# Optimization experiments

Measured on AMD Instinct MI355X. Metric: run time of the kernel, lower is better.

The kernel has to match this reference:

```python
import jax, jax.numpy as jnp
import numpy as np

VIS_DIM, TXT_DIM, HID = 2048, 1024, 1024


def setup_inputs() -> dict:
    key = jax.random.key(0)
    ks = jax.random.split(key, 8)
    def lin(kw, kb, fan_in, fan_out):
        bound = 1.0 / np.sqrt(fan_in)
        W = jax.random.uniform(kw, (fan_out, fan_in), jnp.float32, -bound, bound)
        b = jax.random.uniform(kb, (fan_out,), jnp.float32, -bound, bound)
        return W, b
    Wv, bv = lin(ks[0], ks[1], VIS_DIM, HID)
    Wt, bt = lin(ks[2], ks[3], TXT_DIM, HID)
    Wa, ba = lin(ks[4], ks[5], HID, 1)
    return {
        "visual_features": jax.random.normal(ks[6], (128, 256, VIS_DIM), jnp.float32),
        "text_features": jax.random.normal(ks[7], (128, TXT_DIM), jnp.float32),
        "Wv": Wv, "bv": bv, "Wt": Wt, "bt": bt, "Wa": Wa, "ba": ba,
    }


def reference(visual_features, text_features, Wv, bv, Wt, bt, Wa, ba):
    # v: (B, R, H); t: (B, 1, H) broadcast over regions
    v = jnp.einsum("brd,hd->brh", visual_features, Wv) + bv
    t = (text_features @ Wt.T + bt)[:, None, :]
    combined = jnp.tanh(v + t)                       # (B, R, H)
    scores = jnp.einsum("brh,h->br", combined, Wa[0]) + ba[0]  # (B, R)
    attention_weights = jax.nn.softmax(scores, axis=1)
    attended = jnp.einsum("br,brd->bd", attention_weights, visual_features)
    return attended, attention_weights
```

## Files before the change

kernel.cpp:

```cpp
#include <hip/hip_runtime.h>
#include <hip/hip_bf16.h>

#define VIS_DIM 2048
#define TXT_DIM 1024
#define HID     1024
#define NB      128
#define NR      256
#define M_TOT   (NB*NR)

#define N_ATILES 8192
#define N_TILES  8448
#define TILE_B   16384
#define TSTRIDE  (32 * TILE_B)
#define WS_SCORES_OFF ((size_t)N_TILES * TILE_B)
#define WS_NEED (WS_SCORES_OFF + 131072 + 524288)

typedef __attribute__((ext_vector_type(4))) float  f32x4;
typedef __attribute__((ext_vector_type(8))) short  short8;
typedef __attribute__((ext_vector_type(4))) unsigned short u16x4;

static __device__ __forceinline__ unsigned short f2bf(float f) {
    union { __hip_bfloat16 h; unsigned short u; } c;
    c.h = __float2bfloat16(f);
    return c.u;
}

static __device__ __forceinline__ float bf2f(unsigned short u) {
    union { float f; unsigned u; } c; c.u = ((unsigned)u) << 16; return c.f;
}

static __device__ __forceinline__ float tanh_fast(float x) {
    float xc = fminf(fmaxf(x, -15.f), 15.f);
    float e  = __expf(2.f * xc);
    return (e - 1.f) / (e + 1.f);
}

__global__ void init_ws(float* __restrict__ scores, float* __restrict__ tbuf,
                        const float* __restrict__ bt) {
    int i = blockIdx.x * 256 + threadIdx.x;
    if (i < M_TOT) scores[i] = 0.f;
    tbuf[i] = bt[i & (HID - 1)];
}

__global__ __launch_bounds__(256) void prepass(const float* __restrict__ A,
                                               const float* __restrict__ Bv,
                                               unsigned short* __restrict__ w16) {
    const int t   = blockIdx.x;
    const int tid = threadIdx.x;
    const int mb  = (t < N_ATILES ? t : t - N_ATILES) >> 5;
    const int kt  = t & 31;
    const float* src = (t < N_ATILES ? A : Bv) + (size_t)mb * 128 * VIS_DIM + kt * 64;
    unsigned short* dst = w16 + (size_t)t * (TILE_B / 2);
    #pragma unroll
    for (int i = 0; i < 4; ++i) {
        int si = i * 256 + tid;
        int row = si >> 3, slot = si & 7;
        const float* p = src + (size_t)row * VIS_DIM + slot * 8;
        f32x4 lo = *(const f32x4*)p;
        f32x4 hi = *(const f32x4*)(p + 4);
        short8 v;
        v[0] = (short)f2bf(lo.x); v[1] = (short)f2bf(lo.y);
        v[2] = (short)f2bf(lo.z); v[3] = (short)f2bf(lo.w);
        v[4] = (short)f2bf(hi.x); v[5] = (short)f2bf(hi.y);
        v[6] = (short)f2bf(hi.z); v[7] = (short)f2bf(hi.w);
        *(short8*)(dst + row * 64 + ((slot ^ (row & 7)) << 3)) = v;
    }
}

__global__ __launch_bounds__(256) void gemm_text(const float* __restrict__ text,
                                                 const float* __restrict__ Wt,
                                                 float* __restrict__ tbuf) {
    __shared__ float As[128][33];
    __shared__ float Bs[32][33];
    const int n0  = blockIdx.x * 32;
    const int k0  = blockIdx.y * 256;
    const int tid = threadIdx.x;
    const int tm  = tid >> 3;
    const int tn  = tid & 7;
    float acc[4][4] = {};
    for (int kt = 0; kt < 8; ++kt) {
        const int k = k0 + kt * 32;
        {
            int row = tid >> 1, off = (tid & 1) * 16;
            const float* src = text + row * TXT_DIM + k + off;
            #pragma unroll
            for (int j = 0; j < 4; ++j) {
                f32x4 v = *(const f32x4*)(src + j * 4);
                As[row][off + j*4 + 0] = v.x; As[row][off + j*4 + 1] = v.y;
                As[row][off + j*4 + 2] = v.z; As[row][off + j*4 + 3] = v.w;
            }
        }
        {
            int row = tid >> 3, off = (tid & 7) * 4;
            f32x4 v = *(const f32x4*)(Wt + (size_t)(n0 + row) * TXT_DIM + k + off);
            Bs[row][off + 0] = v.x; Bs[row][off + 1] = v.y;
            Bs[row][off + 2] = v.z; Bs[row][off + 3] = v.w;
        }
        __syncthreads();
        #pragma unroll
        for (int kk = 0; kk < 32; ++kk) {
            float a[4], b[4];
            #pragma unroll
            for (int i = 0; i < 4; ++i) a[i] = As[tm*4 + i][kk];
            #pragma unroll
            for (int j = 0; j < 4; ++j) b[j] = Bs[tn*4 + j][kk];
            #pragma unroll
            for (int i = 0; i < 4; ++i)
                #pragma unroll
                for (int j = 0; j < 4; ++j) acc[i][j] += a[i] * b[j];
        }
        __syncthreads();
    }
    #pragma unroll
    for (int i = 0; i < 4; ++i)
        #pragma unroll
        for (int j = 0; j < 4; ++j)
            atomicAdd(&tbuf[(tm*4 + i) * HID + n0 + tn*4 + j], acc[i][j]);
}

static __device__ __forceinline__ int toff(int row, int kElem) {
    return row * 128 + ((((kElem >> 3) & 7) ^ (row & 7)) << 4);
}

__global__ __launch_bounds__(512, 2) void gemm_256(
        const unsigned short* __restrict__ w16,
        const float* __restrict__ bv,
        const float* __restrict__ wa,
        const float* __restrict__ tbuf,
        float* __restrict__ scores) {
    __shared__ __align__(16) char lds[131072];

    const int wg   = blockIdx.x;
    const int xcd  = wg & 7;
    const int loc  = wg >> 3;
    const int mb   = xcd * 16 + (loc >> 2);
    const int nb   = loc & 3;
    const int brow = mb * 256;
    const int bcol = nb * 256;

    const int tid  = threadIdx.x;
    const int lane = tid & 63;
    const int wid  = tid >> 6;
    const int wr   = wid >> 2;
    const int wc   = wid & 3;
    const int l    = lane & 15, g = lane >> 4;

    const char* wb = (const char*)w16;
    const char* pA = wb + (size_t)(2 * mb) * TSTRIDE + wid * 1024 + lane * 16;
    const char* pB = wb + (size_t)N_ATILES * TILE_B
                        + (size_t)(2 * nb) * TSTRIDE + wid * 1024 + lane * 16;

    f32x4 acc[8][4] = {};

#define GLOADS(koff, bufbase)                                                  \
    do {                                                                       \
        _Pragma("unroll")                                                      \
        for (int j = 0; j < 8; ++j) {                                          \
            const char* s_ = (j < 4                                            \
                ? pA + (j >> 1) * (size_t)TSTRIDE + (j & 1) * 8192             \
                : pB + ((j - 4) >> 1) * (size_t)TSTRIDE + ((j - 4) & 1) * 8192)\
                + (koff);                                                      \
            __builtin_amdgcn_global_load_lds(                                  \
                (const __attribute__((address_space(1))) float*)s_,            \
                (__attribute__((address_space(3))) float*)                     \
                    (lds + (bufbase) + j * 8192 + wid * 1024),                 \
                16, 0, 0);                                                     \
        }                                                                      \
    } while (0)

#define VWAIT0()                                                               \
    do {                                                                       \
        __builtin_amdgcn_sched_barrier(0);                                     \
        asm volatile("s_waitcnt vmcnt(0)" ::: "memory");                       \
        __builtin_amdgcn_sched_barrier(0);                                     \
    } while (0)

#define BARRIER()                                                              \
    do {                                                                       \
        __builtin_amdgcn_sched_barrier(0);                                     \
        asm volatile("s_waitcnt lgkmcnt(0)" ::: "memory");                     \
        __builtin_amdgcn_s_barrier();                                          \
        __builtin_amdgcn_sched_barrier(0);                                     \
    } while (0)

#define PHASE(bufbase, s)                                                      \
    do {                                                                       \
        const int kE = (s) * 32 + g * 8;                                       \
        const char* pa_ = lds + (bufbase) + wr * 16384;                        \
        const char* pb_ = lds + (bufbase) + 32768 + (wc >> 1) * 16384;         \
        short8 bfr[4], afr[8];                                                 \
        _Pragma("unroll")                                                      \
        for (int n = 0; n < 4; ++n)                                            \
            bfr[n] = *(const short8*)(pb_ + toff((wc & 1) * 64 + n * 16 + l, kE)); \
        _Pragma("unroll")                                                      \
        for (int m = 0; m < 8; ++m)                                            \
            afr[m] = *(const short8*)(pa_ + toff(m * 16 + l, kE));             \
        __builtin_amdgcn_s_setprio(1);                                         \
        _Pragma("unroll")                                                      \
        for (int m = 0; m < 8; ++m) {                                          \
            acc[m][0] = __builtin_amdgcn_mfma_f32_16x16x32_bf16(afr[m], bfr[0], acc[m][0], 0, 0, 0); \
            acc[m][1] = __builtin_amdgcn_mfma_f32_16x16x32_bf16(afr[m], bfr[1], acc[m][1], 0, 0, 0); \
            acc[m][2] = __builtin_amdgcn_mfma_f32_16x16x32_bf16(afr[m], bfr[2], acc[m][2], 0, 0, 0); \
            acc[m][3] = __builtin_amdgcn_mfma_f32_16x16x32_bf16(afr[m], bfr[3], acc[m][3], 0, 0, 0); \
        }                                                                      \
        __builtin_amdgcn_s_setprio(0);                                         \
    } while (0)

    GLOADS((size_t)0, 0);
    VWAIT0();
    GLOADS((size_t)TILE_B, 65536);
    BARRIER();

    #pragma unroll 1
    for (int i = 0; i < 16; ++i) {
        const size_t k2 = (size_t)(2 * i + 2) * TILE_B;
        PHASE(0, 0);
        PHASE(0, 1);
        VWAIT0();
        BARRIER();
        if (i < 15) GLOADS(k2, 0);
        PHASE(65536, 0);
        PHASE(65536, 1);
        if (i < 15) {
            VWAIT0();
            BARRIER();
            GLOADS(k2 + TILE_B, 65536);
        }
    }
#undef GLOADS
#undef VWAIT0
#undef BARRIER
#undef PHASE

    const int b = mb;
    float wa_c[4], bvt_c[4];
    #pragma unroll
    for (int n = 0; n < 4; ++n) {
        int col = bcol + wc * 64 + n * 16 + l;
        wa_c[n]  = wa[col];
        bvt_c[n] = bv[col] + tbuf[b * HID + col];
    }
    #pragma unroll
    for (int m = 0; m < 8; ++m) {
        float p0 = 0.f, p1 = 0.f, p2 = 0.f, p3 = 0.f;
        #pragma unroll
        for (int n = 0; n < 4; ++n) {
            f32x4 v = acc[m][n];
            p0 += wa_c[n] * tanh_fast(v.x + bvt_c[n]);
            p1 += wa_c[n] * tanh_fast(v.y + bvt_c[n]);
            p2 += wa_c[n] * tanh_fast(v.z + bvt_c[n]);
            p3 += wa_c[n] * tanh_fast(v.w + bvt_c[n]);
        }
        #pragma unroll
        for (int d = 1; d < 16; d <<= 1) {
            p0 += __shfl_xor(p0, d); p1 += __shfl_xor(p1, d);
            p2 += __shfl_xor(p2, d); p3 += __shfl_xor(p3, d);
        }
        if ((lane & 15) == 0) {
            int rowg = brow + wr * 128 + m * 16 + g * 4;
            atomicAdd(&scores[rowg + 0], p0);
            atomicAdd(&scores[rowg + 1], p1);
            atomicAdd(&scores[rowg + 2], p2);
            atomicAdd(&scores[rowg + 3], p3);
        }
    }
}

__global__ __launch_bounds__(256) void attend_bf16(
        const unsigned short* __restrict__ w16,
        const float* __restrict__ scores,
        float* __restrict__ out) {
    const int chunk = blockIdx.x;
    const int b     = blockIdx.y;
    const int tid   = threadIdx.x;
    const int lane  = tid & 63;
    const int wv    = tid >> 6;

    __shared__ float wsm[NR];
    __shared__ float red[4];
    __shared__ float part2[4][32][8];

    float s = scores[b * NR + tid];
    float mx = s;
    #pragma unroll
    for (int d = 1; d < 64; d <<= 1) mx = fmaxf(mx, __shfl_xor(mx, d));
    if (lane == 0) red[wv] = mx;
    __syncthreads();
    mx = fmaxf(fmaxf(red[0], red[1]), fmaxf(red[2], red[3]));
    float e = __expf(s - mx);
    float sum = e;
    #pragma unroll
    for (int d = 1; d < 64; d <<= 1) sum += __shfl_xor(sum, d);
    __syncthreads();
    if (lane == 0) red[wv] = sum;
    __syncthreads();
    sum = red[0] + red[1] + red[2] + red[3];
    float w = e * (1.f / sum);
    wsm[tid] = w;
    if (chunk == 0) out[(size_t)NB * VIS_DIM + b * NR + tid] = w;
    __syncthreads();

    const int half  = lane >> 5;
    const int dslot = lane & 31;
    const int d0    = chunk * 256 + dslot * 8;
    const int kt    = d0 >> 6;
    const int ksl   = (d0 >> 3) & 7;
    const int rbase = b * 256 + wv * 64 + half;

    float acc[8] = {};
    #pragma unroll 4
    for (int step = 0; step < 32; ++step) {
        int rowg = rbase + step * 2;
        const char* p = (const char*)w16
            + ((size_t)(rowg >> 7) * 32 + kt) * TILE_B
            + (rowg & 127) * 128 + ((ksl ^ (rowg & 7)) << 4);
        short8 v = *(const short8*)p;
        float w_ = wsm[wv * 64 + step * 2 + half];
        #pragma unroll
        for (int j = 0; j < 8; ++j)
            acc[j] += w_ * bf2f((unsigned short)v[j]);
    }
    #pragma unroll
    for (int j = 0; j < 8; ++j) acc[j] += __shfl_xor(acc[j], 32);

    if (half == 0) {
        #pragma unroll
        for (int j = 0; j < 8; ++j) part2[wv][dslot][j] = acc[j];
    }
    __syncthreads();
    if (wv == 0 && half == 0) {
        float o[8];
        #pragma unroll
        for (int j = 0; j < 8; ++j)
            o[j] = part2[0][dslot][j] + part2[1][dslot][j]
                 + part2[2][dslot][j] + part2[3][dslot][j];
        float* dst = out + (size_t)b * VIS_DIM + chunk * 256 + dslot * 8;
        f32x4 lo = {o[0], o[1], o[2], o[3]};
        f32x4 hi = {o[4], o[5], o[6], o[7]};
        *(f32x4*)dst = lo;
        *(f32x4*)(dst + 4) = hi;
    }
}

#define BK 32
#define NT (VIS_DIM / BK)

static __device__ __forceinline__ int tile_off(int row, int kElem) {
    return row * 64 + (((kElem >> 3) ^ ((row >> 1) & 3)) << 4);
}

__global__ __launch_bounds__(256, 2) void gemm_vis(
        const float* __restrict__ A,
        const float* __restrict__ Bv,
        const float* __restrict__ bv,
        const float* __restrict__ wa,
        const float* __restrict__ tbuf,
        float* __restrict__ scores) {
    __shared__ __align__(16) char lds[32768];

    const int wg   = blockIdx.x;
    const int xcd  = wg & 7;
    const int loc  = wg >> 3;
    const int mb   = xcd * 32 + (loc >> 3);
    const int nb   = loc & 7;
    const int brow = mb * 128;
    const int bcol = nb * 128;

    const int tid  = threadIdx.x;
    const int lane = tid & 63;
    const int wid  = tid >> 6;
    const int wr   = wid >> 1, wc = wid & 1;

    const int srow = tid >> 3;
    const int sfs  = tid & 7;
    unsigned va0 = ((unsigned)(brow + srow      ) * VIS_DIM + sfs * 4) * 4u;
    unsigned va1 = va0 + 32u * VIS_DIM * 4u;
    unsigned va2 = va0 + 64u * VIS_DIM * 4u;
    unsigned va3 = va0 + 96u * VIS_DIM * 4u;
    unsigned vb0 = ((unsigned)(bcol + srow      ) * VIS_DIM + sfs * 4) * 4u;
    unsigned vb1 = vb0 + 32u * VIS_DIM * 4u;
    unsigned vb2 = vb0 + 64u * VIS_DIM * 4u;
    unsigned vb3 = vb0 + 96u * VIS_DIM * 4u;

    int wbyte[4];
    #pragma unroll
    for (int r = 0; r < 4; ++r) {
        int row = srow + 32 * r;
        wbyte[r] = row * 64 + (((sfs >> 1) ^ ((row >> 1) & 3)) << 4) + (sfs & 1) * 8;
    }

    f32x4 sA0, sA1, sA2, sA3, sB0, sB1, sB2, sB3;
    f32x4 tA0, tA1, tA2, tA3, tB0, tB1, tB2, tB3;
    f32x4 acc[4][4] = {};

#define GLOAD_SET(dA0,dA1,dA2,dA3,dB0,dB1,dB2,dB3)                             \
    do {                                                                       \
        asm volatile("global_load_dwordx4 %0, %1, %2"                          \
                     : "=&v"(dA0) : "v"(va0), "s"(A) : "memory");              \
        asm volatile("global_load_dwordx4 %0, %1, %2"                          \
                     : "=&v"(dA1) : "v"(va1), "s"(A) : "memory");              \
        asm volatile("global_load_dwordx4 %0, %1, %2"                          \
                     : "=&v"(dA2) : "v"(va2), "s"(A) : "memory");              \
        asm volatile("global_load_dwordx4 %0, %1, %2"                          \
                     : "=&v"(dA3) : "v"(va3), "s"(A) : "memory");              \
        asm volatile("global_load_dwordx4 %0, %1, %2"                          \
                     : "=&v"(dB0) : "v"(vb0), "s"(Bv) : "memory");             \
        asm volatile("global_load_dwordx4 %0, %1, %2"                          \
                     : "=&v"(dB1) : "v"(vb1), "s"(Bv) : "memory");             \
        asm volatile("global_load_dwordx4 %0, %1, %2"                          \
                     : "=&v"(dB2) : "v"(vb2), "s"(Bv) : "memory");             \
        asm volatile("global_load_dwordx4 %0, %1, %2"                          \
                     : "=&v"(dB3) : "v"(vb3), "s"(Bv) : "memory");             \
        va0 += BK * 4; va1 += BK * 4; va2 += BK * 4; va3 += BK * 4;            \
        vb0 += BK * 4; vb1 += BK * 4; vb2 += BK * 4; vb3 += BK * 4;            \
    } while (0)

#define GLOAD_S() GLOAD_SET(sA0,sA1,sA2,sA3,sB0,sB1,sB2,sB3)
#define GLOAD_T() GLOAD_SET(tA0,tA1,tA2,tA3,tB0,tB1,tB2,tB3)

#define VWAIT(N)                                                               \
    do {                                                                       \
        __builtin_amdgcn_sched_barrier(0);                                     \
        asm volatile("s_waitcnt vmcnt(" #N ")" ::: "memory");                  \
        __builtin_amdgcn_sched_barrier(0);                                     \
    } while (0)

#define BARRIER()                                                              \
    do {                                                                       \
        __builtin_amdgcn_sched_barrier(0);                                     \
        asm volatile("s_waitcnt lgkmcnt(0)" ::: "memory");                     \
        __builtin_amdgcn_s_barrier();                                          \
        __builtin_amdgcn_sched_barrier(0);                                     \
    } while (0)

#define CVT8(dst, v0)                                                          \
    do {                                                                       \
        u16x4 t_;                                                              \
        t_.x = f2bf((v0).x); t_.y = f2bf((v0).y);                              \
        t_.z = f2bf((v0).z); t_.w = f2bf((v0).w);                              \
        dst = t_;                                                              \
    } while (0)

#define LWRITE_SET(bufbase, dA0,dA1,dA2,dA3,dB0,dB1,dB2,dB3)                   \
    do {                                                                       \
        u16x4 w_;                                                              \
        char* la = lds + (bufbase);                                            \
        char* lb = lds + (bufbase) + 8192;                                     \
        CVT8(w_, dA0); *(u16x4*)(la + wbyte[0]) = w_;                          \
        CVT8(w_, dA1); *(u16x4*)(la + wbyte[1]) = w_;                          \
        CVT8(w_, dA2); *(u16x4*)(la + wbyte[2]) = w_;                          \
        CVT8(w_, dA3); *(u16x4*)(la + wbyte[3]) = w_;                          \
        CVT8(w_, dB0); *(u16x4*)(lb + wbyte[0]) = w_;                          \
        CVT8(w_, dB1); *(u16x4*)(lb + wbyte[1]) = w_;                          \
        CVT8(w_, dB2); *(u16x4*)(lb + wbyte[2]) = w_;                          \
        CVT8(w_, dB3); *(u16x4*)(lb + wbyte[3]) = w_;                          \
    } while (0)

#define LWRITE_S(bufbase) LWRITE_SET(bufbase, sA0,sA1,sA2,sA3,sB0,sB1,sB2,sB3)
#define LWRITE_T(bufbase) LWRITE_SET(bufbase, tA0,tA1,tA2,tA3,tB0,tB1,tB2,tB3)

#define COMPUTE(bufbase)                                                       \
    do {                                                                       \
        short8 af[4], bf[4];                                                   \
        const int kk = (lane >> 4) * 8;                                        \
        const char* la = lds + (bufbase);                                      \
        const char* lb = lds + (bufbase) + 8192;                               \
        _Pragma("unroll")                                                      \
        for (int m = 0; m < 4; ++m)                                            \
            af[m] = *(const short8*)(la + tile_off(wr*64 + m*16 + (lane&15), kk)); \
        _Pragma("unroll")                                                      \
        for (int n = 0; n < 4; ++n)                                            \
            bf[n] = *(const short8*)(lb + tile_off(wc*64 + n*16 + (lane&15), kk)); \
        _Pragma("unroll")                                                      \
        for (int m = 0; m < 4; ++m)                                            \
            _Pragma("unroll")                                                  \
            for (int n = 0; n < 4; ++n)                                        \
                acc[m][n] = __builtin_amdgcn_mfma_f32_16x16x32_bf16(           \
                    af[m], bf[n], acc[m][n], 0, 0, 0);                         \
    } while (0)

    GLOAD_S();
    GLOAD_T();
    VWAIT(8);
    LWRITE_S(0);
    BARRIER();

    #pragma unroll 1
    for (int kt = 0; kt < NT - 2; kt += 2) {
        GLOAD_S();
        COMPUTE(0);
        VWAIT(8);
        LWRITE_T(16384);
        BARRIER();
        GLOAD_T();
        COMPUTE(16384);
        VWAIT(8);
        LWRITE_S(0);
        BARRIER();
    }
    COMPUTE(0);
    VWAIT(0);
    LWRITE_T(16384);
    BARRIER();
    COMPUTE(16384);
#undef GLOAD_SET
#undef GLOAD_S
#undef GLOAD_T
#undef VWAIT
#undef BARRIER
#undef CVT8
#undef LWRITE_SET
#undef LWRITE_S
#undef LWRITE_T
#undef COMPUTE

    const int b = brow >> 8;
    float wa_c[4], bvt_c[4];
    #pragma unroll
    for (int n = 0; n < 4; ++n) {
        int col = bcol + wc * 64 + n * 16 + (lane & 15);
        wa_c[n]  = wa[col];
        bvt_c[n] = bv[col] + tbuf[b * HID + col];
    }
    #pragma unroll
    for (int m = 0; m < 4; ++m) {
        float p0 = 0.f, p1 = 0.f, p2 = 0.f, p3 = 0.f;
        #pragma unroll
        for (int n = 0; n < 4; ++n) {
            f32x4 v = acc[m][n];
            p0 += wa_c[n] * tanh_fast(v.x + bvt_c[n]);
            p1 += wa_c[n] * tanh_fast(v.y + bvt_c[n]);
            p2 += wa_c[n] * tanh_fast(v.z + bvt_c[n]);
            p3 += wa_c[n] * tanh_fast(v.w + bvt_c[n]);
        }
        #pragma unroll
        for (int d = 1; d < 16; d <<= 1) {
            p0 += __shfl_xor(p0, d); p1 += __shfl_xor(p1, d);
            p2 += __shfl_xor(p2, d); p3 += __shfl_xor(p3, d);
        }
        if ((lane & 15) == 0) {
            int rowg = brow + wr * 64 + m * 16 + (lane >> 4) * 4;
            atomicAdd(&scores[rowg + 0], p0);
            atomicAdd(&scores[rowg + 1], p1);
            atomicAdd(&scores[rowg + 2], p2);
            atomicAdd(&scores[rowg + 3], p3);
        }
    }
}

__global__ __launch_bounds__(256) void attend(const float* __restrict__ visual,
                                              const float* __restrict__ scores,
                                              float* __restrict__ out) {
    const int chunk = blockIdx.x;
    const int b     = blockIdx.y;
    const int tid   = threadIdx.x;
    const int lane  = tid & 63;
    const int wv    = tid >> 6;

    __shared__ float wsm[NR];
    __shared__ float red[4];
    __shared__ f32x4 part[4][64];

    float s = scores[b * NR + tid];
    float mx = s;
    #pragma unroll
    for (int d = 1; d < 64; d <<= 1) mx = fmaxf(mx, __shfl_xor(mx, d));
    if (lane == 0) red[wv] = mx;
    __syncthreads();
    mx = fmaxf(fmaxf(red[0], red[1]), fmaxf(red[2], red[3]));
    float e = __expf(s - mx);
    float sum = e;
    #pragma unroll
    for (int d = 1; d < 64; d <<= 1) sum += __shfl_xor(sum, d);
    __syncthreads();
    if (lane == 0) red[wv] = sum;
    __syncthreads();
    sum = red[0] + red[1] + red[2] + red[3];
    float w = e * (1.f / sum);
    wsm[tid] = w;
    if (chunk == 0) out[(size_t)NB * VIS_DIM + b * NR + tid] = w;
    __syncthreads();

    const float* vb = visual + ((size_t)b * NR + wv * 64) * VIS_DIM + chunk * 256 + lane * 4;
    f32x4 acc = {0.f, 0.f, 0.f, 0.f};
    #pragma unroll
    for (int r = 0; r < 64; r += 4) {
        f32x4 v0 = *(const f32x4*)(vb + (size_t)(r + 0) * VIS_DIM);
        f32x4 v1 = *(const f32x4*)(vb + (size_t)(r + 1) * VIS_DIM);
        f32x4 v2 = *(const f32x4*)(vb + (size_t)(r + 2) * VIS_DIM);
        f32x4 v3 = *(const f32x4*)(vb + (size_t)(r + 3) * VIS_DIM);
        acc += wsm[wv * 64 + r + 0] * v0;
        acc += wsm[wv * 64 + r + 1] * v1;
        acc += wsm[wv * 64 + r + 2] * v2;
        acc += wsm[wv * 64 + r + 3] * v3;
    }
    part[wv][lane] = acc;
    __syncthreads();
    if (wv == 0) {
        f32x4 a = part[0][lane] + part[1][lane] + part[2][lane] + part[3][lane];
        *(f32x4*)(out + (size_t)b * VIS_DIM + chunk * 256 + lane * 4) = a;
    }
}

extern "C" void kernel_launch(void* const* d_in, const int* in_sizes, int n_in,
                              void* d_out, int out_size, void* d_ws, size_t ws_size,
                              hipStream_t stream) {
    (void)in_sizes; (void)n_in; (void)out_size;
    const float* visual = (const float*)d_in[0];
    const float* text   = (const float*)d_in[1];
    const float* Wv     = (const float*)d_in[2];
    const float* bv     = (const float*)d_in[3];
    const float* Wt     = (const float*)d_in[4];
    const float* bt     = (const float*)d_in[5];
    const float* Wa     = (const float*)d_in[6];

    float* out = (float*)d_out;
    const bool fast = ws_size >= (size_t)WS_NEED;

    if (fast) {
        unsigned short* w16 = (unsigned short*)d_ws;
        float* scores = (float*)((char*)d_ws + WS_SCORES_OFF);
        float* tbuf   = scores + M_TOT;
        prepass    <<<N_TILES, 256, 0, stream>>>(visual, Wv, w16);
        init_ws    <<<512, 256, 0, stream>>>(scores, tbuf, bt);
        gemm_text  <<<dim3(32, 4), 256, 0, stream>>>(text, Wt, tbuf);
        gemm_256   <<<512, 512, 0, stream>>>(w16, bv, Wa, tbuf, scores);
        attend_bf16<<<dim3(8, NB), 256, 0, stream>>>(w16, scores, out);
    } else {
        float* scores = (float*)d_ws;
        float* tbuf   = scores + M_TOT;
        init_ws  <<<512, 256, 0, stream>>>(scores, tbuf, bt);
        gemm_text<<<dim3(32, 4), 256, 0, stream>>>(text, Wt, tbuf);
        gemm_vis <<<2048, 256, 0, stream>>>(visual, Wv, bv, Wa, tbuf, scores);
        attend   <<<dim3(8, NB), 256, 0, stream>>>(visual, scores, out);
    }
}
```

Measured before the change: 247.3 us.

## Split MFMA phases into half-tiles with ping-pong barriers around compute

Restructures the main GEMM loop into 32 iterations, each split into four sub-phases that handle half of the M fragments (4 rows of MFMA tiles). Every sub-phase is bracketed by workgroup barriers, and B fragments are reused across the two M halves. The aim is to interleave LDS reads and MFMA across waves, ping-pong style, while cutting live A-fragment registers. The cost is many more s_barrier calls per tile, which could add synchronization stalls.

```diff
diff --git a/kernel.cpp b/kernel.cpp
--- a/kernel.cpp
+++ b/kernel.cpp
@@ -183,27 +183,36 @@
         __builtin_amdgcn_sched_barrier(0);                                     \
     } while (0)
 
-#define PHASE(bufbase, s)                                                      \
+#define PH(bufbase, s, mh, LOADBF, LAST)                                       \
     do {                                                                       \
         const int kE = (s) * 32 + g * 8;                                       \
         const char* pa_ = lds + (bufbase) + wr * 16384;                        \
         const char* pb_ = lds + (bufbase) + 32768 + (wc >> 1) * 16384;         \
-        short8 bfr[4], afr[8];                                                 \
+        if (LOADBF) {                                                          \
+            _Pragma("unroll")                                                  \
+            for (int n = 0; n < 4; ++n)                                        \
+                bfr[n] = *(const short8*)(pb_ + toff((wc & 1) * 64 + n * 16 + l, kE)); \
+        }                                                                      \
         _Pragma("unroll")                                                      \
-        for (int n = 0; n < 4; ++n)                                            \
-            bfr[n] = *(const short8*)(pb_ + toff((wc & 1) * 64 + n * 16 + l, kE)); \
-        _Pragma("unroll")                                                      \
-        for (int m = 0; m < 8; ++m)                                            \
-            afr[m] = *(const short8*)(pa_ + toff(m * 16 + l, kE));             \
+        for (int m = 0; m < 4; ++m)                                            \
+            afr[m] = *(const short8*)(pa_ + toff((mh) * 64 + m * 16 + l, kE)); \
+        __builtin_amdgcn_sched_barrier(0);                                     \
+        __builtin_amdgcn_s_barrier();                                          \
+        asm volatile("s_waitcnt lgkmcnt(0)" ::: "memory");                     \
+        __builtin_amdgcn_sched_barrier(0);                                     \
         __builtin_amdgcn_s_setprio(1);                                         \
         _Pragma("unroll")                                                      \
-        for (int m = 0; m < 8; ++m) {                                          \
-            acc[m][0] = __builtin_amdgcn_mfma_f32_16x16x32_bf16(afr[m], bfr[0], acc[m][0], 0, 0, 0); \
-            acc[m][1] = __builtin_amdgcn_mfma_f32_16x16x32_bf16(afr[m], bfr[1], acc[m][1], 0, 0, 0); \
-            acc[m][2] = __builtin_amdgcn_mfma_f32_16x16x32_bf16(afr[m], bfr[2], acc[m][2], 0, 0, 0); \
-            acc[m][3] = __builtin_amdgcn_mfma_f32_16x16x32_bf16(afr[m], bfr[3], acc[m][3], 0, 0, 0); \
+        for (int m = 0; m < 4; ++m) {                                          \
+            acc[(mh)*4+m][0] = __builtin_amdgcn_mfma_f32_16x16x32_bf16(afr[m], bfr[0], acc[(mh)*4+m][0], 0, 0, 0); \
+            acc[(mh)*4+m][1] = __builtin_amdgcn_mfma_f32_16x16x32_bf16(afr[m], bfr[1], acc[(mh)*4+m][1], 0, 0, 0); \
+            acc[(mh)*4+m][2] = __builtin_amdgcn_mfma_f32_16x16x32_bf16(afr[m], bfr[2], acc[(mh)*4+m][2], 0, 0, 0); \
+            acc[(mh)*4+m][3] = __builtin_amdgcn_mfma_f32_16x16x32_bf16(afr[m], bfr[3], acc[(mh)*4+m][3], 0, 0, 0); \
         }                                                                      \
         __builtin_amdgcn_s_setprio(0);                                         \
+        __builtin_amdgcn_sched_barrier(0);                                     \
+        if (LAST) { asm volatile("s_waitcnt vmcnt(0)" ::: "memory"); }         \
+        __builtin_amdgcn_s_barrier();                                          \
+        __builtin_amdgcn_sched_barrier(0);                                     \
     } while (0)
 
     GLOADS((size_t)0, 0);
@@ -212,25 +221,19 @@
     BARRIER();
 
     #pragma unroll 1
-    for (int i = 0; i < 16; ++i) {
-        const size_t k2 = (size_t)(2 * i + 2) * TILE_B;
-        PHASE(0, 0);
-        PHASE(0, 1);
-        VWAIT0();
-        BARRIER();
-        if (i < 15) GLOADS(k2, 0);
-        PHASE(65536, 0);
-        PHASE(65536, 1);
-        if (i < 15) {
-            VWAIT0();
-            BARRIER();
-            GLOADS(k2 + TILE_B, 65536);
-        }
+    for (int t = 0; t < 32; ++t) {
+        const int bn = (t & 1) << 16;
+        short8 bfr[4], afr[4];
+        PH(bn, 0, 0, 1, 0);
+        PH(bn, 0, 1, 0, 0);
+        PH(bn, 1, 0, 1, 0);
+        PH(bn, 1, 1, 0, 1);
+        if (t < 30) GLOADS((size_t)(t + 2) * TILE_B, bn);
     }
 #undef GLOADS
 #undef VWAIT0
 #undef BARRIER
-#undef PHASE
+#undef PH
 
     const int b = mb;
     float wa_c[4], bvt_c[4];
```

New measurement: 271.5 us. 9.8% more time.
